# Optimization experiments

Hardware: AMD Instinct MI355X
Metric: run time of the kernel (lower is better)

Reference implementation:

```python
import jax, jax.numpy as jnp
import numpy as np

L_IN, L_ENC, B = 1024, 1024, 16
D_IN, D_ENC, D_EMB = 512, 512, 512


def setup_inputs() -> dict:
    key = jax.random.key(0)
    ks = jax.random.split(key, 9)
    s_in = 1.0 / np.sqrt(D_IN)
    s_emb = 1.0 / np.sqrt(D_EMB)
    s_enc = 1.0 / np.sqrt(D_ENC)
    return {
        "in_seq": jax.random.normal(ks[0], (L_IN, B, D_IN), jnp.float32),
        "enc_seq": jax.random.normal(ks[1], (L_ENC, B, D_ENC), jnp.float32),
        "prev_target_seq": jax.random.normal(ks[2], (L_IN, B, D_EMB), jnp.float32),
        # torch Linear weights: (out_features, in_features)
        "W_in2enc": jax.random.normal(ks[3], (D_ENC, D_IN), jnp.float32) * s_in,
        "b_in2enc": jnp.zeros((D_ENC,), jnp.float32),
        "W_lab2enc": jax.random.normal(ks[4], (D_ENC, D_EMB), jnp.float32) * s_emb,
        "b_lab2enc": jnp.zeros((D_ENC,), jnp.float32),
        "W_enc2in": jax.random.normal(ks[5], (D_IN, D_ENC), jnp.float32) * s_enc,
        "b_enc2in": jnp.zeros((D_IN,), jnp.float32),
    }


def reference(in_seq, enc_seq, prev_target_seq,
              W_in2enc, b_in2enc, W_lab2enc, b_lab2enc, W_enc2in, b_enc2in):
    # d_vals: (L_in, B, D_enc) = proj(in_seq) + proj(prev_target_seq)
    in_proj = jnp.einsum('lbi,ei->lbe', in_seq, W_in2enc) + b_in2enc
    tgt_proj = jnp.einsum('lbm,em->lbe', prev_target_seq, W_lab2enc) + b_lab2enc
    d_vals = in_proj + tgt_proj
    # raw attention scores: (L_in, L_enc, B) dot products over D_enc
    scores = jnp.einsum('lbe,mbe->lmb', d_vals, enc_seq)
    # sum-normalization (NOT softmax) over the encoder-length axis
    attn = scores / jnp.sum(scores, axis=1, keepdims=True)
    # weighted sum of encoder states: (L_in, B, D_enc)
    context = jnp.einsum('lmb,mbe->lbe', attn, enc_seq)
    # project back to input dim
    return jnp.einsum('lbe,ie->lbi', context, W_enc2in) + b_enc2in
```

## Files before the change

### kernel.cpp

```cpp
#include <hip/hip_runtime.h>
#include <cstdint>

static constexpr int LDR = 8192;

typedef uint16_t u16;
typedef __attribute__((ext_vector_type(8))) short short8;
typedef __attribute__((ext_vector_type(4))) float f32x4;
struct alignas(8) U16x4 { u16 x, y, z, w; };

__device__ __forceinline__ u16 f2bf(float f) {
    union { float f; unsigned u; } v; v.f = f;
    unsigned r = v.u + 0x7fffu + ((v.u >> 16) & 1u);
    return (u16)(r >> 16);
}

__device__ __forceinline__ short8 cvt8(const float4 a, const float4 b) {
    short8 r;
    r[0]=(short)f2bf(a.x); r[1]=(short)f2bf(a.y); r[2]=(short)f2bf(a.z); r[3]=(short)f2bf(a.w);
    r[4]=(short)f2bf(b.x); r[5]=(short)f2bf(b.y); r[6]=(short)f2bf(b.z); r[7]=(short)f2bf(b.w);
    return r;
}

__device__ __forceinline__ void gl_lds16(const u16* g, unsigned ldsaddr) {
    asm volatile("s_mov_b32 m0, %0\n\t"
                 "global_load_lds_dwordx4 %1, off"
                 :: "s"(__builtin_amdgcn_readfirstlane(ldsaddr)), "v"(g)
                 : "memory");
}

template<int MODE>
__global__ __launch_bounds__(256) void gemm_async(
    const u16* __restrict__ A, const u16* __restrict__ Bm,
    const float* __restrict__ b1, const float* __restrict__ b2,
    const float* __restrict__ b3, const float* __restrict__ Sinv,
    u16* __restrict__ Cb, float* __restrict__ Cf)
{
    constexpr int K   = (MODE == 1 || MODE == 5) ? 1024 : 512;
    constexpr int BM  = (MODE == 5 || MODE == 6) ? 64 : 128;
    constexpr int NJ  = (BM == 128) ? 4 : 2;
    constexpr int NIA = BM / 32;
    constexpr int NIB = 4;
    constexpr int ASZ = BM * 128;
    constexpr int BSZ = 128 * 128;
    constexpr int LDA = (MODE == 1) ? 1024 : (MODE == 4) ? 8192 : (MODE == 5) ? 1024 : 512;
    constexpr int LDB = (MODE == 1 || MODE == 5) ? 1024 : 512;

    __shared__ __align__(16) u16 lds[(2*ASZ + 2*BSZ) / 2];

    const int z    = blockIdx.z;
    const int row0 = blockIdx.y * BM;
    const int col0 = blockIdx.x * 128;
    const int tid  = threadIdx.x;
    const int l    = tid & 63, w = tid >> 6;
    const int wm   = (BM == 128) ? (w >> 1) : 0;
    const int wn   = (BM == 128) ? (w & 1) : w;
    const int quad = l >> 4, l16 = l & 15;

    const u16* Ab = A;
    const u16* Bb = Bm;
    if constexpr (MODE == 4) Ab = A + z*512;
    if constexpr (MODE == 5) { Ab = A + z*524288; Bb = Bm + z*524288; }
    if constexpr (MODE == 6) Bb = Bm + z*262144;
    if constexpr (MODE == 4) Bb = Bm + z*262144;

    const int lq = l >> 3;
    const int loffu = ((l & 7) ^ lq) * 8;
    const u16* gA[NIA];
    #pragma unroll
    for (int i = 0; i < NIA; ++i)
        gA[i] = Ab + (size_t)(row0 + i*32 + w*8 + lq) * LDA + loffu;
    const u16* gB[NIB];
    #pragma unroll
    for (int i = 0; i < NIB; ++i)
        gB[i] = Bb + (size_t)(col0 + i*32 + w*8 + lq) * LDB + loffu;

    const unsigned lbase = (unsigned)(size_t)&lds[0];

    auto stage = [&](int c) {
        #pragma unroll
        for (int i = 0; i < NIA; ++i) {
            gl_lds16(gA[i], lbase + c*ASZ + i*4096 + w*1024);
            gA[i] += 64;
        }
        #pragma unroll
        for (int i = 0; i < NIB; ++i) {
            gl_lds16(gB[i], lbase + 2*ASZ + c*BSZ + i*4096 + w*1024);
            gB[i] += 64;
        }
    };

    f32x4 acc[4][NJ] = {};
    const int swzr = (l16 & 7) << 3;
    const int arow = wm * 64;
    const int brow = wn * (BM == 128 ? 64 : 32);

    stage(0);
    int cur = 0;
    for (int kb = 0; kb < K; kb += 64) {
        asm volatile("s_waitcnt vmcnt(0)" ::: "memory");
        __syncthreads();
        if (kb + 64 < K) stage(cur ^ 1);
        const int abase = cur * (ASZ/2);
        const int bbase = ASZ + cur * (BSZ/2);
        #pragma unroll
        for (int kk = 0; kk < 2; ++kk) {
            const int koff = (kk*32 + quad*8) ^ swzr;
            short8 af[4], bfr[NJ];
            #pragma unroll
            for (int i = 0; i < 4; ++i)
                af[i] = *(const short8*)&lds[abase + (arow + i*16 + l16)*64 + koff];
            #pragma unroll
            for (int j = 0; j < NJ; ++j)
                bfr[j] = *(const short8*)&lds[bbase + (brow + j*16 + l16)*64 + koff];
            #pragma unroll
            for (int i = 0; i < 4; ++i)
                #pragma unroll
                for (int j = 0; j < NJ; ++j)
                    acc[i][j] = __builtin_amdgcn_mfma_f32_16x16x32_bf16(af[i], bfr[j], acc[i][j], 0, 0, 0);
        }
        cur ^= 1;
    }

    #pragma unroll
    for (int i = 0; i < 4; ++i) {
        const int grow = row0 + arow + i*16 + quad*4;
        #pragma unroll
        for (int j = 0; j < NJ; ++j) {
            const int gcol = col0 + brow + j*16 + l16;
            #pragma unroll
            for (int r = 0; r < 4; ++r) {
                float v = acc[i][j][r];
                const int R = grow + r;
                if constexpr (MODE == 1) {
                    v += b1[gcol] + b2[gcol];
                    Cb[R*512 + gcol] = f2bf(v);
                } else if constexpr (MODE == 5 || MODE == 6) {
                    Cb[z*262144 + R*512 + gcol] = f2bf(v);
                } else {
                    const float s = Sinv[R*16 + z];
                    Cf[(R*16 + z)*512 + gcol] = v * s + b3[gcol];
                }
            }
        }
    }
}

__global__ __launch_bounds__(256) void enct_kernel(
    const float* __restrict__ E, u16* __restrict__ EncT, double* __restrict__ part)
{
    __shared__ float tile[64][65];
    __shared__ double sred[256];
    const int bb = blockIdx.z;
    const int m0 = blockIdx.y * 64;
    const int e0 = blockIdx.x * 64;
    const int t = threadIdx.x;
    const int tr = t >> 4;
    const int tc4 = (t & 15) * 4;
    #pragma unroll
    for (int it = 0; it < 4; ++it) {
        const int ml = tr + it*16;
        float4 v = *(const float4*)&E[(m0+ml)*LDR + bb*512 + e0 + tc4];
        *(float4*)&tile[ml][tc4] = v;
    }
    __syncthreads();
    #pragma unroll
    for (int it = 0; it < 4; ++it) {
        const int el = tr + it*16;
        U16x4 o;
        o.x = f2bf(tile[tc4+0][el]);
        o.y = f2bf(tile[tc4+1][el]);
        o.z = f2bf(tile[tc4+2][el]);
        o.w = f2bf(tile[tc4+3][el]);
        *(U16x4*)&EncT[bb*524288 + (e0+el)*1024 + m0 + tc4] = o;
    }
    const int el = t & 63, mq = t >> 6;
    double a = 0.0;
    #pragma unroll
    for (int j = 0; j < 16; ++j) a += (double)tile[mq*16 + j][el];
    sred[t] = a;
    __syncthreads();
    if (t < 64) {
        double s = sred[t] + sred[t+64] + sred[t+128] + sred[t+192];
        part[blockIdx.y*8192 + bb*512 + e0 + t] = s;
    }
}

__global__ __launch_bounds__(256) void prep_small(
    const float* __restrict__ W1, const float* __restrict__ W2,
    const float* __restrict__ W3, const float* __restrict__ b1,
    const float* __restrict__ b2, const double* __restrict__ part,
    u16* __restrict__ W12, u16* __restrict__ W3b,
    double* __restrict__ u, double* __restrict__ cd)
{
    const int blk = blockIdx.x, tid = threadIdx.x;
    if (blk < 384) {
        const int idx = blk*256 + tid;
        if (idx < 65536) {
            const int r = idx >> 7, k8 = (idx & 127) * 8;
            const float* src = (k8 < 512) ? (W1 + r*512 + k8) : (W2 + r*512 + (k8 - 512));
            float4 a = *(const float4*)src;
            float4 b = *((const float4*)src + 1);
            *(short8*)&W12[r*1024 + k8] = cvt8(a, b);
        } else {
            const int i2 = idx - 65536;
            const int r = i2 >> 6, k8 = (i2 & 63) * 8;
            const float* src = W3 + r*512 + k8;
            float4 a = *(const float4*)src;
            float4 b = *((const float4*)src + 1);
            *(short8*)&W3b[r*512 + k8] = cvt8(a, b);
        }
        return;
    }
    __shared__ double es_l[512];
    __shared__ double red[256];
    int b;
    if (blk < 448) b = ((blk - 384) & 31) >> 1;
    else           b = blk - 448;
    for (int e = tid; e < 512; e += 256) {
        double s = 0.0;
        #pragma unroll
        for (int c = 0; c < 16; ++c) s += part[c*8192 + b*512 + e];
        es_l[e] = s;
    }
    __syncthreads();
    if (blk < 448) {
        const int blk2 = blk - 384;
        const int which = blk2 >> 5;
        const int t = (blk2 & 31)*256 + tid;
        const int i = t & 511;
        const float* W = which ? W2 : W1;
        double a = 0.0;
        for (int e = 0; e < 512; ++e) a += (double)W[e*512 + i] * es_l[e];
        u[which*8192 + t] = a;
    } else {
        double a = 0.0;
        for (int e = tid; e < 512; e += 256) a += (double)(b1[e] + b2[e]) * es_l[e];
        red[tid] = a; __syncthreads();
        for (int s = 128; s > 0; s >>= 1) { if (tid < s) red[tid] += red[tid+s]; __syncthreads(); }
        if (tid == 0) cd[b] = red[0];
    }
}

__global__ __launch_bounds__(256) void s_xt_kernel(
    const float* __restrict__ X, const float* __restrict__ T,
    const double* __restrict__ u, const double* __restrict__ cd,
    float* __restrict__ Sinv, u16* __restrict__ XT)
{
    const int wave = threadIdx.x >> 6, lane = threadIdx.x & 63;
    const int b = blockIdx.x & 15, g = blockIdx.x >> 4;
    const int e = lane * 8;
    double u1r[8], u2r[8];
    #pragma unroll
    for (int k = 0; k < 8; ++k) {
        u1r[k] = u[b*512 + e + k];
        u2r[k] = u[8192 + b*512 + e + k];
    }
    const double cb = cd[b];
    #pragma unroll 2
    for (int i = 0; i < 8; ++i) {
        const int j = g*32 + wave*8 + i;
        const int r = j*16 + b;
        float4 x0 = *(const float4*)&X[r*512 + e];
        float4 x1 = *(const float4*)&X[r*512 + e + 4];
        float4 t0 = *(const float4*)&T[r*512 + e];
        float4 t1 = *(const float4*)&T[r*512 + e + 4];
        double a = 0.0;
        a += (double)x0.x*u1r[0] + (double)x0.y*u1r[1] + (double)x0.z*u1r[2] + (double)x0.w*u1r[3];
        a += (double)x1.x*u1r[4] + (double)x1.y*u1r[5] + (double)x1.z*u1r[6] + (double)x1.w*u1r[7];
        a += (double)t0.x*u2r[0] + (double)t0.y*u2r[1] + (double)t0.z*u2r[2] + (double)t0.w*u2r[3];
        a += (double)t1.x*u2r[4] + (double)t1.y*u2r[5] + (double)t1.z*u2r[6] + (double)t1.w*u2r[7];
        *(short8*)&XT[r*1024 + e]       = cvt8(x0, x1);
        *(short8*)&XT[r*1024 + 512 + e] = cvt8(t0, t1);
        #pragma unroll
        for (int off = 32; off > 0; off >>= 1) a += __shfl_down(a, off, 64);
        if (lane == 0) Sinv[r] = (float)(1.0 / (a + cb));
    }
}

extern "C" void kernel_launch(void* const* d_in, const int* in_sizes, int n_in,
                              void* d_out, int out_size, void* d_ws, size_t ws_size,
                              hipStream_t stream)
{
    const float* X   = (const float*)d_in[0];
    const float* Enc = (const float*)d_in[1];
    const float* T   = (const float*)d_in[2];
    const float* W1  = (const float*)d_in[3];
    const float* b1  = (const float*)d_in[4];
    const float* W2  = (const float*)d_in[5];
    const float* b2  = (const float*)d_in[6];
    const float* W3  = (const float*)d_in[7];
    const float* b3  = (const float*)d_in[8];
    float* out = (float*)d_out;

    char* w = (char*)d_ws;
    u16*    dvals_bf = (u16*)(w);
    u16*    EncT_bf  = (u16*)(w + 16777216);
    u16*    Gram_bf  = (u16*)(w + 33554432);
    u16*    HT_bf    = (u16*)(w + 41943040);
    u16*    W12      = (u16*)(w + 50331648);
    u16*    W3b      = (u16*)(w + 51380224);
    double* part     = (double*)(w + 51904512);
    double* u        = (double*)(w + 52953088);
    double* cd       = (double*)(w + 53084160);
    float*  Sinv     = (float*)(w + 53084288);
    u16*    XTb      = (u16*)d_out;

    dim3 blk(256);
    enct_kernel <<<dim3(8, 16, 16), blk, 0, stream>>>(Enc, EncT_bf, part);
    prep_small  <<<dim3(464),       blk, 0, stream>>>(W1, W2, W3, b1, b2, part, W12, W3b, u, cd);
    s_xt_kernel <<<dim3(512),       blk, 0, stream>>>(X, T, u, cd, Sinv, XTb);

    gemm_async<5><<<dim3(4, 8, 16),  blk, 0, stream>>>(EncT_bf, EncT_bf, b1, b2, b3, Sinv, Gram_bf, out);
    gemm_async<6><<<dim3(4, 8, 16),  blk, 0, stream>>>(W3b, Gram_bf, b1, b2, b3, Sinv, HT_bf, out);
    gemm_async<1><<<dim3(4, 128, 1), blk, 0, stream>>>(XTb, W12, b1, b2, b3, Sinv, dvals_bf, out);
    gemm_async<4><<<dim3(4, 8, 16),  blk, 0, stream>>>(dvals_bf, HT_bf, b1, b2, b3, Sinv, dvals_bf, out);
}
```

Baseline: 247.6 us.

## Use triple-buffered 64-row GEMM tiles with batch-grouped d_vals layout

Makes every GEMM mode use 64x128 tiles with a three-stage LDS ring, waiting only on the older stage's loads (vmcnt(6)) so two K-blocks of global loads stay in flight. The MFMA section runs at raised wave priority. The d_vals GEMM now writes its output regrouped by batch, so the final attention GEMM reads contiguous rows with stride 512 instead of stride 8192. Grids double in the row dimension, which trades more blocks and less per-block reuse for better latency hiding and occupancy, at the cost of larger LDS use per block.

```diff
diff --git a/kernel.cpp b/kernel.cpp
--- a/kernel.cpp
+++ b/kernel.cpp
@@ -35,105 +35,100 @@
     const float* __restrict__ b3, const float* __restrict__ Sinv,
     u16* __restrict__ Cb, float* __restrict__ Cf)
 {
-    constexpr int K   = (MODE == 1 || MODE == 5) ? 1024 : 512;
-    constexpr int BM  = (MODE == 5 || MODE == 6) ? 64 : 128;
-    constexpr int NJ  = (BM == 128) ? 4 : 2;
-    constexpr int NIA = BM / 32;
-    constexpr int NIB = 4;
-    constexpr int ASZ = BM * 128;
-    constexpr int BSZ = 128 * 128;
-    constexpr int LDA = (MODE == 1) ? 1024 : (MODE == 4) ? 8192 : (MODE == 5) ? 1024 : 512;
-    constexpr int LDB = (MODE == 1 || MODE == 5) ? 1024 : 512;
-
-    __shared__ __align__(16) u16 lds[(2*ASZ + 2*BSZ) / 2];
+    constexpr int K    = (MODE == 1 || MODE == 5) ? 1024 : 512;
+    constexpr int LDA  = (MODE == 1 || MODE == 5) ? 1024 : 512;
+    constexpr int LDB  = (MODE == 1 || MODE == 5) ? 1024 : 512;
+    constexpr int ABUF = 64 * 128;
+    constexpr int BBUF = 128 * 128;
+    constexpr int BUF  = ABUF + BBUF;
+
+    __shared__ __align__(16) u16 lds[3 * BUF / 2];
 
     const int z    = blockIdx.z;
-    const int row0 = blockIdx.y * BM;
+    const int row0 = blockIdx.y * 64;
     const int col0 = blockIdx.x * 128;
     const int tid  = threadIdx.x;
     const int l    = tid & 63, w = tid >> 6;
-    const int wm   = (BM == 128) ? (w >> 1) : 0;
-    const int wn   = (BM == 128) ? (w & 1) : w;
     const int quad = l >> 4, l16 = l & 15;
 
     const u16* Ab = A;
     const u16* Bb = Bm;
-    if constexpr (MODE == 4) Ab = A + z*512;
     if constexpr (MODE == 5) { Ab = A + z*524288; Bb = Bm + z*524288; }
-    if constexpr (MODE == 6) Bb = Bm + z*262144;
-    if constexpr (MODE == 4) Bb = Bm + z*262144;
+    if constexpr (MODE == 6) { Bb = Bm + z*262144; }
+    if constexpr (MODE == 4) { Ab = A + z*524288; Bb = Bm + z*262144; }
 
     const int lq = l >> 3;
     const int loffu = ((l & 7) ^ lq) * 8;
-    const u16* gA[NIA];
-    #pragma unroll
-    for (int i = 0; i < NIA; ++i)
+    const u16* gA[2];
+    #pragma unroll
+    for (int i = 0; i < 2; ++i)
         gA[i] = Ab + (size_t)(row0 + i*32 + w*8 + lq) * LDA + loffu;
-    const u16* gB[NIB];
-    #pragma unroll
-    for (int i = 0; i < NIB; ++i)
+    const u16* gB[4];
+    #pragma unroll
+    for (int i = 0; i < 4; ++i)
         gB[i] = Bb + (size_t)(col0 + i*32 + w*8 + lq) * LDB + loffu;
 
     const unsigned lbase = (unsigned)(size_t)&lds[0];
 
-    auto stage = [&](int c) {
-        #pragma unroll
-        for (int i = 0; i < NIA; ++i) {
-            gl_lds16(gA[i], lbase + c*ASZ + i*4096 + w*1024);
+    auto stage = [&](unsigned bufb) {
+        #pragma unroll
+        for (int i = 0; i < 2; ++i) {
+            gl_lds16(gA[i], lbase + bufb + i*4096 + w*1024);
             gA[i] += 64;
         }
         #pragma unroll
-        for (int i = 0; i < NIB; ++i) {
-            gl_lds16(gB[i], lbase + 2*ASZ + c*BSZ + i*4096 + w*1024);
+        for (int i = 0; i < 4; ++i) {
+            gl_lds16(gB[i], lbase + bufb + ABUF + i*4096 + w*1024);
             gB[i] += 64;
         }
     };
 
-    f32x4 acc[4][NJ] = {};
+    f32x4 acc[4][2] = {};
     const int swzr = (l16 & 7) << 3;
-    const int arow = wm * 64;
-    const int brow = wn * (BM == 128 ? 64 : 32);
-
-    stage(0);
-    int cur = 0;
+
+    stage(0); stage(BUF);
+    unsigned buf0 = 0, buf1 = BUF, buf2 = 2*BUF;
     for (int kb = 0; kb < K; kb += 64) {
-        asm volatile("s_waitcnt vmcnt(0)" ::: "memory");
+        if (kb + 64 < K) asm volatile("s_waitcnt vmcnt(6)" ::: "memory");
+        else             asm volatile("s_waitcnt vmcnt(0)" ::: "memory");
         __syncthreads();
-        if (kb + 64 < K) stage(cur ^ 1);
-        const int abase = cur * (ASZ/2);
-        const int bbase = ASZ + cur * (BSZ/2);
+        if (kb + 128 < K) stage(buf2);
+        const int abase = buf0 / 2;
+        const int bbase = buf0 / 2 + ABUF / 2;
+        __builtin_amdgcn_s_setprio(1);
         #pragma unroll
         for (int kk = 0; kk < 2; ++kk) {
             const int koff = (kk*32 + quad*8) ^ swzr;
-            short8 af[4], bfr[NJ];
+            short8 af[4], bfr[2];
             #pragma unroll
             for (int i = 0; i < 4; ++i)
-                af[i] = *(const short8*)&lds[abase + (arow + i*16 + l16)*64 + koff];
+                af[i] = *(const short8*)&lds[abase + (i*16 + l16)*64 + koff];
             #pragma unroll
-            for (int j = 0; j < NJ; ++j)
-                bfr[j] = *(const short8*)&lds[bbase + (brow + j*16 + l16)*64 + koff];
+            for (int j = 0; j < 2; ++j)
+                bfr[j] = *(const short8*)&lds[bbase + (w*32 + j*16 + l16)*64 + koff];
             #pragma unroll
             for (int i = 0; i < 4; ++i)
                 #pragma unroll
-                for (int j = 0; j < NJ; ++j)
+                for (int j = 0; j < 2; ++j)
                     acc[i][j] = __builtin_amdgcn_mfma_f32_16x16x32_bf16(af[i], bfr[j], acc[i][j], 0, 0, 0);
         }
-        cur ^= 1;
+        __builtin_amdgcn_s_setprio(0);
+        unsigned tmp = buf0; buf0 = buf1; buf1 = buf2; buf2 = tmp;
     }
 
     #pragma unroll
     for (int i = 0; i < 4; ++i) {
-        const int grow = row0 + arow + i*16 + quad*4;
-        #pragma unroll
-        for (int j = 0; j < NJ; ++j) {
-            const int gcol = col0 + brow + j*16 + l16;
+        const int grow = row0 + i*16 + quad*4;
+        #pragma unroll
+        for (int j = 0; j < 2; ++j) {
+            const int gcol = col0 + w*32 + j*16 + l16;
             #pragma unroll
             for (int r = 0; r < 4; ++r) {
                 float v = acc[i][j][r];
                 const int R = grow + r;
                 if constexpr (MODE == 1) {
                     v += b1[gcol] + b2[gcol];
-                    Cb[R*512 + gcol] = f2bf(v);
+                    Cb[((R & 15)*1024 + (R >> 4))*512 + gcol] = f2bf(v);
                 } else if constexpr (MODE == 5 || MODE == 6) {
                     Cb[z*262144 + R*512 + gcol] = f2bf(v);
                 } else {
@@ -293,7 +288,7 @@
     float* out = (float*)d_out;
 
     char* w = (char*)d_ws;
-    u16*    dvals_bf = (u16*)(w);
+    u16*    dvals_g  = (u16*)(w);
     u16*    EncT_bf  = (u16*)(w + 16777216);
     u16*    Gram_bf  = (u16*)(w + 33554432);
     u16*    HT_bf    = (u16*)(w + 41943040);
@@ -312,6 +307,6 @@
 
     gemm_async<5><<<dim3(4, 8, 16),  blk, 0, stream>>>(EncT_bf, EncT_bf, b1, b2, b3, Sinv, Gram_bf, out);
     gemm_async<6><<<dim3(4, 8, 16),  blk, 0, stream>>>(W3b, Gram_bf, b1, b2, b3, Sinv, HT_bf, out);
-    gemm_async<1><<<dim3(4, 128, 1), blk, 0, stream>>>(XTb, W12, b1, b2, b3, Sinv, dvals_bf, out);
-    gemm_async<4><<<dim3(4, 8, 16),  blk, 0, stream>>>(dvals_bf, HT_bf, b1, b2, b3, Sinv, dvals_bf, out);
-}
+    gemm_async<1><<<dim3(4, 256, 1), blk, 0, stream>>>(XTb, W12, b1, b2, b3, Sinv, dvals_g, out);
+    gemm_async<4><<<dim3(4, 16, 16), blk, 0, stream>>>(dvals_g, HT_bf, b1, b2, b3, Sinv, dvals_g, out);
+}
```

Result: no change. 252.3 us (+1.9%).
